# Kernel optimization log

Measured on AMD Instinct MI355X. Metric: run time of the kernel, lower is better.

Reference implementation:

```python
import jax, jax.numpy as jnp
import numpy as np
from jax import lax

B, N, D = 4, 2048, 1024
MAX_SEQ = 2048
GROUPS = 4  # math.gcd(1024, 4)
LN_EPS = 1e-5


def setup_inputs() -> dict:
    key = jax.random.key(0)
    ks = jax.random.split(key, 12)
    s = 0.02
    return {
        "x": jax.random.normal(ks[0], (B, N, D), jnp.float32),
        "Wq": jax.random.normal(ks[1], (D, D), jnp.float32) * s,
        "Wk": jax.random.normal(ks[2], (D, D), jnp.float32) * s,
        "Wv": jax.random.normal(ks[3], (D, D), jnp.float32) * s,
        "rel_bias": jax.random.normal(ks[4], (1, MAX_SEQ, MAX_SEQ), jnp.float32) * s,
        "conv_w": jax.random.normal(ks[5], (D, D // GROUPS, 3), jnp.float32) * s,
        "conv_b": jnp.zeros((D,), jnp.float32),
        "resg_w": jax.random.normal(ks[6], (D, D), jnp.float32) * s,
        "resg_b": jnp.zeros((D,), jnp.float32),
        "ln_g": jnp.ones((D,), jnp.float32),
        "ln_b": jnp.zeros((D,), jnp.float32),
        "fc1_w": jax.random.normal(ks[7], (D // 2, D), jnp.float32) * s,
        "fc1_b": jnp.zeros((D // 2,), jnp.float32),
        "fc2_w": jax.random.normal(ks[8], (1, D // 2), jnp.float32) * s,
        "fc2_b": jnp.zeros((1,), jnp.float32),
    }


def _forward(x, Wq, Wk, Wv, rel_bias, conv_w, conv_b, resg_w, resg_b,
             ln_g, ln_b, fc1_w, fc1_b, fc2_w, fc2_b):
    b, n, d = x.shape
    scale = 1.0 / jnp.sqrt(jnp.asarray(d, x.dtype))
    q = x @ Wq.T  # [b,n,dk]
    k = x @ Wk.T
    v = x @ Wv.T  # [b,n,dv]
    att = jnp.einsum("bqd,bkd->bqk", q, k) * scale + rel_bias[:, :n, :n]
    causal = jnp.tril(jnp.ones((n, n), bool))
    att = jnp.where(causal, att, jnp.asarray(-jnp.inf, att.dtype))
    att = jax.nn.softmax(att, axis=-1)  # dropout is identity at eval
    att_out = jnp.einsum("bqk,bkd->bqd", att, v)
    # grouped temporal conv over sequence dim: v [b,n,dv] -> NCH [b,dv,n]
    conv = lax.conv_general_dilated(
        v.transpose(0, 2, 1), conv_w, window_strides=(1,), padding=[(1, 1)],
        dimension_numbers=("NCH", "OIH", "NCH"), feature_group_count=GROUPS)
    conv = conv + conv_b[None, :, None]
    out = att_out + conv.transpose(0, 2, 1)
    res = jax.nn.sigmoid(out @ resg_w.T + resg_b)
    out = x + res * out
    mu = out.mean(-1, keepdims=True)
    var = out.var(-1, keepdims=True)
    out = (out - mu) * lax.rsqrt(var + LN_EPS) * ln_g + ln_b
    h = jax.nn.gelu(out @ fc1_w.T + fc1_b, approximate=False)
    return jax.nn.sigmoid(h @ fc2_w.T + fc2_b)


def reference(x, Wq, Wk, Wv, rel_bias, conv_w, conv_b, resg_w, resg_b,
              ln_g, ln_b, fc1_w, fc1_b, fc2_w, fc2_b):
    return _forward(x, Wq, Wk, Wv, rel_bias, conv_w, conv_b, resg_w, resg_b,
                    ln_g, ln_b, fc1_w, fc1_b, fc2_w, fc2_b)
```

## Files before the change

kernel.cpp:

```cpp
#include <hip/hip_runtime.h>
#include <math.h>

#define NSEQ 2048
#define DDIM 1024
#define BSZ  4
#define BM 128
#define BN 128
#define BK 32

typedef short bf16x8 __attribute__((ext_vector_type(8)));
typedef float f32x4 __attribute__((ext_vector_type(4)));
typedef unsigned int u32;
typedef unsigned short u16;

__device__ __forceinline__ u16 f2bf(float f) {
  union { float f; u32 u; } x; x.f = f;
  u32 r = x.u + 0x7FFFu + ((x.u >> 16) & 1u);
  return (u16)(r >> 16);
}
__device__ __forceinline__ float bf2f(u16 h) {
  union { u32 u; float f; } x; x.u = ((u32)h) << 16; return x.f;
}
__device__ __forceinline__ float sigmoidf_(float x) {
  return 1.0f / (1.0f + expf(-x));
}

__device__ __forceinline__ void async_copy16(const u16* g, u16* l) {
  __builtin_amdgcn_global_load_lds(
      (const __attribute__((address_space(1))) u32*)g,
      (__attribute__((address_space(3))) u32*)l, 16, 0, 0);
}

__device__ __forceinline__ void stage_tile(const u16* __restrict__ gsrc, size_t ld,
                                           int k0, u16* lds, int tid) {
  const int wave = tid >> 6, lane = tid & 63;
  const int rr = lane >> 2, cc = (lane & 3) << 3;
#pragma unroll
  for (int j = 0; j < 2; ++j) {
    const int c = j * 4 + wave;
    async_copy16(gsrc + (size_t)(c * 16 + rr) * ld + k0 + cc, lds + c * 512);
  }
}

__device__ __forceinline__ void mfma_step(const u16* Al, const u16* Bl,
                                          int wr, int wc, int l16, int quad,
                                          f32x4 acc[4][4]) {
  bf16x8 a[4], b[4];
#pragma unroll
  for (int i = 0; i < 4; ++i) {
    a[i] = *(const bf16x8*)(Al + (wr * 64 + i * 16 + l16) * BK + quad * 8);
    b[i] = *(const bf16x8*)(Bl + (wc * 64 + i * 16 + l16) * BK + quad * 8);
  }
#pragma unroll
  for (int i = 0; i < 4; ++i)
#pragma unroll
    for (int j = 0; j < 4; ++j)
      acc[i][j] = __builtin_amdgcn_mfma_f32_16x16x32_bf16(a[i], b[j], acc[i][j], 0, 0, 0);
}

__device__ __forceinline__ void zero_acc(f32x4 acc[4][4]) {
#pragma unroll
  for (int i = 0; i < 4; ++i)
#pragma unroll
    for (int j = 0; j < 4; ++j) {
      f32x4 z = {0.f, 0.f, 0.f, 0.f};
      acc[i][j] = z;
    }
}

__device__ __forceinline__ void gemm_loop(const u16* A, size_t lda,
                                          const u16* Bt, size_t ldb, int K,
                                          u16* Al, u16* Bl, int tid,
                                          int wr, int wc, int l16, int quad,
                                          f32x4 acc[4][4]) {
  for (int k0 = 0; k0 < K; k0 += BK) {
    __syncthreads();
    stage_tile(A, lda, k0, Al, tid);
    stage_tile(Bt, ldb, k0, Bl, tid);
    __syncthreads();
    mfma_step(Al, Bl, wr, wc, l16, quad, acc);
  }
}

__global__ __launch_bounds__(256) void k_cvt(const float* __restrict__ s,
                                             u16* __restrict__ d, int n4) {
  const int i = blockIdx.x * 256 + threadIdx.x;
  if (i < n4) {
    const float4 v = ((const float4*)s)[i];
    ushort4 o;
    o.x = f2bf(v.x); o.y = f2bf(v.y); o.z = f2bf(v.z); o.w = f2bf(v.w);
    ((ushort4*)d)[i] = o;
  }
}

__global__ __launch_bounds__(256) void k_cvtconv(const float* __restrict__ s,
                                                 u16* __restrict__ d) {
  const int o = blockIdx.x, i = threadIdx.x;
#pragma unroll
  for (int tap = 0; tap < 3; ++tap)
    d[(size_t)o * 768 + tap * 256 + i] = f2bf(s[(size_t)o * 768 + i * 3 + tap]);
}

__global__ __launch_bounds__(256) void k_zeropad(u16* __restrict__ vpad) {
  const int bb = blockIdx.x >> 1, which = blockIdx.x & 1;
  u16* row = vpad + (size_t)bb * 2050 * 1024 + (which ? (size_t)2049 * 1024 : 0);
  ushort4 z = {0, 0, 0, 0};
  ((ushort4*)row)[threadIdx.x] = z;
}

__global__ __launch_bounds__(256) void k_qkv(
    const u16* __restrict__ xb, const u16* __restrict__ Wqb,
    const u16* __restrict__ Wkb, const u16* __restrict__ Wvb,
    u16* __restrict__ qb, u16* __restrict__ kb, u16* __restrict__ vpad)
{
  __shared__ u16 Al[BM * BK], Bl[BN * BK];
  const int tid = threadIdx.x, z = blockIdx.z;
  const u16* W = (z == 0) ? Wqb : ((z == 1) ? Wkb : Wvb);
  const int row0 = blockIdx.x * BM, col0 = blockIdx.y * BN;
  const int lane = tid & 63, wave = tid >> 6;
  const int quad = lane >> 4, l16 = lane & 15, wr = wave >> 1, wc = wave & 1;
  f32x4 acc[4][4];
  zero_acc(acc);
  gemm_loop(xb + (size_t)row0 * DDIM, DDIM, W + (size_t)col0 * DDIM, DDIM, DDIM,
            Al, Bl, tid, wr, wc, l16, quad, acc);
#pragma unroll
  for (int mi = 0; mi < 4; ++mi)
#pragma unroll
    for (int r = 0; r < 4; ++r) {
      const int grow = row0 + wr * 64 + mi * 16 + quad * 4 + r;
#pragma unroll
      for (int ni = 0; ni < 4; ++ni) {
        const int gcol = col0 + wc * 64 + ni * 16 + l16;
        const u16 hv = f2bf(acc[mi][ni][r]);
        if (z == 2) {
          const int b = grow >> 11, t = grow & 2047;
          vpad[(size_t)b * 2050 * 1024 + 1024 + (size_t)t * 1024 + gcol] = hv;
        } else {
          (z == 0 ? qb : kb)[(size_t)grow * DDIM + gcol] = hv;
        }
      }
    }
}

__global__ __launch_bounds__(256) void k_vt(const u16* __restrict__ vpad,
                                            u16* __restrict__ vT)
{
  __shared__ u16 tile[64][72];
  const int t0 = blockIdx.x * 64, d0 = blockIdx.y * 64, b = blockIdx.z;
  const int tid = threadIdx.x;
  const u16* vb = vpad + (size_t)b * 2050 * 1024 + 1024;
#pragma unroll
  for (int p = 0; p < 4; ++p) {
    const int r = p * 16 + (tid >> 4), c = (tid & 15) << 2;
    const ushort4 v4 = *(const ushort4*)(vb + (size_t)(t0 + r) * 1024 + d0 + c);
    tile[r][c] = v4.x; tile[r][c + 1] = v4.y; tile[r][c + 2] = v4.z; tile[r][c + 3] = v4.w;
  }
  __syncthreads();
  u16* ob = vT + (size_t)b * DDIM * NSEQ;
#pragma unroll
  for (int p = 0; p < 4; ++p) {
    const int d = p * 16 + (tid >> 4), t = (tid & 15) << 2;
    ushort4 o;
    o.x = tile[t][d]; o.y = tile[t + 1][d]; o.z = tile[t + 2][d]; o.w = tile[t + 3][d];
    *(ushort4*)(ob + (size_t)(d0 + d) * NSEQ + t0 + t) = o;
  }
}

__global__ __launch_bounds__(256) void k_scores(
    const u16* __restrict__ qb, const u16* __restrict__ kb,
    const float* __restrict__ rb, u16* __restrict__ att)
{
  const int it = blockIdx.x, jt = blockIdx.y, b = blockIdx.z;
  if (jt > it) return;
  __shared__ u16 Al[BM * BK], Bl[BN * BK];
  const int tid = threadIdx.x;
  const int row0 = it * BM, col0 = jt * BN;
  const int lane = tid & 63, wave = tid >> 6;
  const int quad = lane >> 4, l16 = lane & 15, wr = wave >> 1, wc = wave & 1;
  f32x4 acc[4][4];
  zero_acc(acc);
  gemm_loop(qb + ((size_t)b * NSEQ + row0) * DDIM, DDIM,
            kb + ((size_t)b * NSEQ + col0) * DDIM, DDIM, DDIM,
            Al, Bl, tid, wr, wc, l16, quad, acc);
  u16* abase = att + (size_t)b * NSEQ * NSEQ;
#pragma unroll
  for (int mi = 0; mi < 4; ++mi)
#pragma unroll
    for (int r = 0; r < 4; ++r) {
      const int i = row0 + wr * 64 + mi * 16 + quad * 4 + r;
#pragma unroll
      for (int ni = 0; ni < 4; ++ni) {
        const int j = col0 + wc * 64 + ni * 16 + l16;
        abase[(size_t)i * NSEQ + j] =
            f2bf(acc[mi][ni][r] * 0.03125f + rb[(size_t)i * NSEQ + j]);
      }
    }
}

__global__ __launch_bounds__(256) void k_softmax(u16* __restrict__ att)
{
  const int i = blockIdx.x, b = blockIdx.y;
  u16* row = att + ((size_t)b * NSEQ + i) * NSEQ;
  const int valid = i + 1;
  const int wlen = ((i >> 7) + 1) << 7;
  const int tid = threadIdx.x;
  const int lane = tid & 63, wid = tid >> 6;

  float v[8];
  float m = -1e30f;
#pragma unroll
  for (int t = 0; t < 8; ++t) {
    const int idx = tid + (t << 8);
    v[t] = (idx < valid) ? bf2f(row[idx]) : -1e30f;
    m = fmaxf(m, v[t]);
  }
#pragma unroll
  for (int off = 32; off; off >>= 1) m = fmaxf(m, __shfl_xor(m, off));
  __shared__ float red[4];
  if (lane == 0) red[wid] = m;
  __syncthreads();
  m = fmaxf(fmaxf(red[0], red[1]), fmaxf(red[2], red[3]));
  __syncthreads();

  float s = 0.f;
#pragma unroll
  for (int t = 0; t < 8; ++t) {
    const int idx = tid + (t << 8);
    float e = (idx < valid) ? expf(v[t] - m) : 0.f;
    v[t] = e;
    s += e;
  }
#pragma unroll
  for (int off = 32; off; off >>= 1) s += __shfl_xor(s, off);
  if (lane == 0) red[wid] = s;
  __syncthreads();
  s = red[0] + red[1] + red[2] + red[3];
  const float inv = 1.0f / s;
#pragma unroll
  for (int t = 0; t < 8; ++t) {
    const int idx = tid + (t << 8);
    if (idx < wlen) row[idx] = f2bf(v[t] * inv);
  }
}

__global__ __launch_bounds__(256) void k_pv(
    const u16* __restrict__ att, const u16* __restrict__ vT,
    float* __restrict__ buf1)
{
  __shared__ u16 Al[BM * BK], Bl[BN * BK];
  const int it = blockIdx.x, nt = blockIdx.y, b = blockIdx.z;
  const int tid = threadIdx.x;
  const int row0 = it * BM, col0 = nt * BN;
  const int K = (it + 1) * BM;
  const int lane = tid & 63, wave = tid >> 6;
  const int quad = lane >> 4, l16 = lane & 15, wr = wave >> 1, wc = wave & 1;
  f32x4 acc[4][4];
  zero_acc(acc);
  gemm_loop(att + ((size_t)b * NSEQ + row0) * NSEQ, NSEQ,
            vT + ((size_t)b * DDIM + col0) * NSEQ, NSEQ, K,
            Al, Bl, tid, wr, wc, l16, quad, acc);
  float* obase = buf1 + (size_t)b * NSEQ * DDIM;
#pragma unroll
  for (int mi = 0; mi < 4; ++mi)
#pragma unroll
    for (int r = 0; r < 4; ++r) {
      const int grow = row0 + wr * 64 + mi * 16 + quad * 4 + r;
#pragma unroll
      for (int ni = 0; ni < 4; ++ni) {
        const int gcol = col0 + wc * 64 + ni * 16 + l16;
        obase[(size_t)grow * DDIM + gcol] = acc[mi][ni][r];
      }
    }
}

__global__ __launch_bounds__(256) void k_conv(
    const u16* __restrict__ vpad, const u16* __restrict__ cwp,
    const float* __restrict__ cb, float* __restrict__ buf1,
    u16* __restrict__ buf1b)
{
  __shared__ u16 Al[BM * BK], Bl[BN * BK];
  const int tid = threadIdx.x;
  const int row0 = blockIdx.x * BM;
  const int col0 = blockIdx.y * BN;
  const int g = col0 >> 8;
  const int b = row0 >> 11, t0 = row0 & 2047;
  const u16* vb = vpad + (size_t)b * 2050 * 1024 + 1024;
  const u16* Bbase = cwp + (size_t)col0 * 768;
  const int lane = tid & 63, wave = tid >> 6;
  const int quad = lane >> 4, l16 = lane & 15, wr = wave >> 1, wc = wave & 1;
  const int rr = lane >> 2, cc = (lane & 3) << 3;
  const int gch = g << 8;
  f32x4 acc[4][4];
  zero_acc(acc);
  for (int k0 = 0; k0 < 768; k0 += BK) {
    __syncthreads();
    const int tap = k0 >> 8;
    const int i0 = k0 & 255;
#pragma unroll
    for (int j = 0; j < 2; ++j) {
      const int c = j * 4 + wave;
      const int r = c * 16 + rr;
      async_copy16(vb + (size_t)(t0 + r - 1 + tap) * 1024 + gch + i0 + cc,
                   Al + c * 512);
    }
    stage_tile(Bbase, 768, k0, Bl, tid);
    __syncthreads();
    mfma_step(Al, Bl, wr, wc, l16, quad, acc);
  }
#pragma unroll
  for (int mi = 0; mi < 4; ++mi)
#pragma unroll
    for (int r = 0; r < 4; ++r) {
      const int grow = row0 + wr * 64 + mi * 16 + quad * 4 + r;
#pragma unroll
      for (int ni = 0; ni < 4; ++ni) {
        const int gcol = col0 + wc * 64 + ni * 16 + l16;
        const size_t idx = (size_t)grow * DDIM + gcol;
        const float val = buf1[idx] + cb[gcol] + acc[mi][ni][r];
        buf1[idx] = val;
        buf1b[idx] = f2bf(val);
      }
    }
}

__global__ __launch_bounds__(256) void k_resgate(
    const u16* __restrict__ buf1b, const u16* __restrict__ rwb,
    const float* __restrict__ rbias, const float* __restrict__ x,
    const float* __restrict__ buf1, float* __restrict__ buf2)
{
  __shared__ u16 Al[BM * BK], Bl[BN * BK];
  const int tid = threadIdx.x;
  const int row0 = blockIdx.x * BM, col0 = blockIdx.y * BN;
  const int lane = tid & 63, wave = tid >> 6;
  const int quad = lane >> 4, l16 = lane & 15, wr = wave >> 1, wc = wave & 1;
  f32x4 acc[4][4];
  zero_acc(acc);
  gemm_loop(buf1b + (size_t)row0 * DDIM, DDIM, rwb + (size_t)col0 * DDIM, DDIM,
            DDIM, Al, Bl, tid, wr, wc, l16, quad, acc);
#pragma unroll
  for (int mi = 0; mi < 4; ++mi)
#pragma unroll
    for (int r = 0; r < 4; ++r) {
      const int grow = row0 + wr * 64 + mi * 16 + quad * 4 + r;
#pragma unroll
      for (int ni = 0; ni < 4; ++ni) {
        const int gcol = col0 + wc * 64 + ni * 16 + l16;
        const size_t idx = (size_t)grow * DDIM + gcol;
        const float gate = sigmoidf_(acc[mi][ni][r] + rbias[gcol]);
        buf2[idx] = x[idx] + gate * buf1[idx];
      }
    }
}

__global__ __launch_bounds__(256) void k_ln(
    const float* __restrict__ buf, const float* __restrict__ gw,
    const float* __restrict__ gb, u16* __restrict__ outb)
{
  const int row = blockIdx.x;
  const float* p = buf + (size_t)row * DDIM;
  const int tid = threadIdx.x;
  const int lane = tid & 63, wid = tid >> 6;
  const int c = tid << 2;
  float4 val = *(const float4*)(p + c);
  float s = val.x + val.y + val.z + val.w;
  float s2 = val.x * val.x + val.y * val.y + val.z * val.z + val.w * val.w;
#pragma unroll
  for (int off = 32; off; off >>= 1) {
    s += __shfl_xor(s, off);
    s2 += __shfl_xor(s2, off);
  }
  __shared__ float r1[4], r2[4];
  if (lane == 0) { r1[wid] = s; r2[wid] = s2; }
  __syncthreads();
  s = r1[0] + r1[1] + r1[2] + r1[3];
  s2 = r2[0] + r2[1] + r2[2] + r2[3];
  const float mean = s * (1.0f / DDIM);
  const float var = s2 * (1.0f / DDIM) - mean * mean;
  const float rstd = rsqrtf(var + 1e-5f);
  const float4 g4 = *(const float4*)(gw + c);
  const float4 b4 = *(const float4*)(gb + c);
  ushort4 o;
  o.x = f2bf((val.x - mean) * rstd * g4.x + b4.x);
  o.y = f2bf((val.y - mean) * rstd * g4.y + b4.y);
  o.z = f2bf((val.z - mean) * rstd * g4.z + b4.z);
  o.w = f2bf((val.w - mean) * rstd * g4.w + b4.w);
  *(ushort4*)(outb + (size_t)row * DDIM + c) = o;
}

__global__ __launch_bounds__(256) void k_fc1(
    const u16* __restrict__ A, const u16* __restrict__ W,
    const float* __restrict__ bias, float* __restrict__ h)
{
  __shared__ u16 Al[BM * BK], Bl[BN * BK];
  const int tid = threadIdx.x;
  const int row0 = blockIdx.x * BM, col0 = blockIdx.y * BN;
  const int lane = tid & 63, wave = tid >> 6;
  const int quad = lane >> 4, l16 = lane & 15, wr = wave >> 1, wc = wave & 1;
  f32x4 acc[4][4];
  zero_acc(acc);
  gemm_loop(A + (size_t)row0 * DDIM, DDIM, W + (size_t)col0 * DDIM, DDIM, DDIM,
            Al, Bl, tid, wr, wc, l16, quad, acc);
#pragma unroll
  for (int mi = 0; mi < 4; ++mi)
#pragma unroll
    for (int r = 0; r < 4; ++r) {
      const int grow = row0 + wr * 64 + mi * 16 + quad * 4 + r;
#pragma unroll
      for (int ni = 0; ni < 4; ++ni) {
        const int gcol = col0 + wc * 64 + ni * 16 + l16;
        const float t = acc[mi][ni][r] + bias[gcol];
        h[(size_t)grow * 512 + gcol] = 0.5f * t * (1.0f + erff(t * 0.70710678118654752f));
      }
    }
}

__global__ __launch_bounds__(256) void k_fc2(
    const float* __restrict__ h, const float* __restrict__ w,
    const float* __restrict__ b2, float* __restrict__ out)
{
  const int r = blockIdx.x * 4 + (threadIdx.x >> 6);
  const int lane = threadIdx.x & 63;
  const float* hp = h + (size_t)r * 512;
  float s = 0.f;
#pragma unroll
  for (int t = 0; t < 8; ++t) {
    const int c = lane + t * 64;
    s = fmaf(hp[c], w[c], s);
  }
#pragma unroll
  for (int off = 32; off; off >>= 1) s += __shfl_xor(s, off);
  if (lane == 0) out[r] = sigmoidf_(s + b2[0]);
}

extern "C" void kernel_launch(void* const* d_in, const int* in_sizes, int n_in,
                              void* d_out, int out_size, void* d_ws, size_t ws_size,
                              hipStream_t stream) {
  const float* x    = (const float*)d_in[0];
  const float* Wq   = (const float*)d_in[1];
  const float* Wk   = (const float*)d_in[2];
  const float* Wv   = (const float*)d_in[3];
  const float* rb   = (const float*)d_in[4];
  const float* cw   = (const float*)d_in[5];
  const float* cb   = (const float*)d_in[6];
  const float* rw   = (const float*)d_in[7];
  const float* rbias= (const float*)d_in[8];
  const float* lng  = (const float*)d_in[9];
  const float* lnb  = (const float*)d_in[10];
  const float* f1w  = (const float*)d_in[11];
  const float* f1b  = (const float*)d_in[12];
  const float* f2w  = (const float*)d_in[13];
  const float* f2b  = (const float*)d_in[14];
  float* out = (float*)d_out;
  char* w8 = (char*)d_ws;

  u16* xb    = (u16*)(w8 + 0);
  u16* Wqb   = (u16*)(w8 + 16777216);
  u16* Wkb   = (u16*)(w8 + 18874368);
  u16* Wvb   = (u16*)(w8 + 20971520);
  u16* rwb   = (u16*)(w8 + 23068672);
  u16* f1wb  = (u16*)(w8 + 25165824);
  u16* cwp   = (u16*)(w8 + 26214400);
  u16* qb    = (u16*)(w8 + 27787264);
  u16* kb    = (u16*)(w8 + 44564480);
  u16* vpad  = (u16*)(w8 + 61341696);
  u16* vT    = (u16*)(w8 + 78131200);
  u16* att   = (u16*)(w8 + 94908416);
  float* buf1  = (float*)(w8 + 27787264);
  u16*   buf1b = (u16*)(w8 + 0);
  float* buf2  = (float*)(w8 + 94908416);
  u16*   ln16  = (u16*)(w8 + 78131200);
  float* h     = (float*)(w8 + 61341696);

  k_zeropad<<<dim3(8),    256, 0, stream>>>(vpad);
  k_cvt    <<<dim3(8192), 256, 0, stream>>>(x,   xb,   2097152);
  k_cvt    <<<dim3(1024), 256, 0, stream>>>(Wq,  Wqb,  262144);
  k_cvt    <<<dim3(1024), 256, 0, stream>>>(Wk,  Wkb,  262144);
  k_cvt    <<<dim3(1024), 256, 0, stream>>>(Wv,  Wvb,  262144);
  k_cvt    <<<dim3(1024), 256, 0, stream>>>(rw,  rwb,  262144);
  k_cvt    <<<dim3(512),  256, 0, stream>>>(f1w, f1wb, 131072);
  k_cvtconv<<<dim3(1024), 256, 0, stream>>>(cw, cwp);

  k_qkv    <<<dim3(64, 8, 3),  256, 0, stream>>>(xb, Wqb, Wkb, Wvb, qb, kb, vpad);
  k_vt     <<<dim3(32, 16, 4), 256, 0, stream>>>(vpad, vT);
  k_scores <<<dim3(16, 16, 4), 256, 0, stream>>>(qb, kb, rb, att);
  k_softmax<<<dim3(NSEQ, BSZ), 256, 0, stream>>>(att);
  k_pv     <<<dim3(16, 8, 4),  256, 0, stream>>>(att, vT, buf1);
  k_conv   <<<dim3(64, 8),     256, 0, stream>>>(vpad, cwp, cb, buf1, buf1b);
  k_resgate<<<dim3(64, 8),     256, 0, stream>>>(buf1b, rwb, rbias, x, buf1, buf2);
  k_ln     <<<dim3(BSZ * NSEQ),256, 0, stream>>>(buf2, lng, lnb, ln16);
  k_fc1    <<<dim3(64, 4),     256, 0, stream>>>(ln16, f1wb, f1b, h);
  k_fc2    <<<dim3(NSEQ),      256, 0, stream>>>(h, f2w, f2b, out);
}
```

Before: 444.8 us.

## Swizzle LDS tiles, merge prep kernels, keep attention scores in fp32

Applies an XOR swizzle to the k-group column used when staging tiles into LDS and when reading MFMA operands, so lanes spread across LDS banks instead of conflicting. Merges the seven conversion and zero-pad launches into one k_prep kernel to cut launch overhead. Stores the pre-softmax scores as fp32, presumably for accuracy, and writes bf16 probabilities to a separate buffer. That doubles the score write and read traffic and needs a reorganized workspace layout.

Measured after the change: 415.8 us. 1.07x faster.

```diff
diff --git a/kernel.cpp b/kernel.cpp
--- a/kernel.cpp
+++ b/kernel.cpp
@@ -34,7 +34,9 @@
 __device__ __forceinline__ void stage_tile(const u16* __restrict__ gsrc, size_t ld,
                                            int k0, u16* lds, int tid) {
   const int wave = tid >> 6, lane = tid & 63;
-  const int rr = lane >> 2, cc = (lane & 3) << 3;
+  const int rr = lane >> 2;
+  const int kg = (lane & 3) ^ ((lane >> 3) & 3);
+  const int cc = kg << 3;
 #pragma unroll
   for (int j = 0; j < 2; ++j) {
     const int c = j * 4 + wave;
@@ -45,11 +47,12 @@
 __device__ __forceinline__ void mfma_step(const u16* Al, const u16* Bl,
                                           int wr, int wc, int l16, int quad,
                                           f32x4 acc[4][4]) {
+  const int qs = (quad ^ ((l16 >> 1) & 3)) << 3;
   bf16x8 a[4], b[4];
 #pragma unroll
   for (int i = 0; i < 4; ++i) {
-    a[i] = *(const bf16x8*)(Al + (wr * 64 + i * 16 + l16) * BK + quad * 8);
-    b[i] = *(const bf16x8*)(Bl + (wc * 64 + i * 16 + l16) * BK + quad * 8);
+    a[i] = *(const bf16x8*)(Al + (wr * 64 + i * 16 + l16) * BK + qs);
+    b[i] = *(const bf16x8*)(Bl + (wc * 64 + i * 16 + l16) * BK + qs);
   }
 #pragma unroll
   for (int i = 0; i < 4; ++i)
@@ -82,30 +85,41 @@
   }
 }
 
-__global__ __launch_bounds__(256) void k_cvt(const float* __restrict__ s,
-                                             u16* __restrict__ d, int n4) {
-  const int i = blockIdx.x * 256 + threadIdx.x;
-  if (i < n4) {
-    const float4 v = ((const float4*)s)[i];
-    ushort4 o;
-    o.x = f2bf(v.x); o.y = f2bf(v.y); o.z = f2bf(v.z); o.w = f2bf(v.w);
-    ((ushort4*)d)[i] = o;
-  }
-}
-
-__global__ __launch_bounds__(256) void k_cvtconv(const float* __restrict__ s,
-                                                 u16* __restrict__ d) {
-  const int o = blockIdx.x, i = threadIdx.x;
-#pragma unroll
-  for (int tap = 0; tap < 3; ++tap)
-    d[(size_t)o * 768 + tap * 256 + i] = f2bf(s[(size_t)o * 768 + i * 3 + tap]);
-}
-
-__global__ __launch_bounds__(256) void k_zeropad(u16* __restrict__ vpad) {
-  const int bb = blockIdx.x >> 1, which = blockIdx.x & 1;
-  u16* row = vpad + (size_t)bb * 2050 * 1024 + (which ? (size_t)2049 * 1024 : 0);
-  ushort4 z = {0, 0, 0, 0};
-  ((ushort4*)row)[threadIdx.x] = z;
+__global__ __launch_bounds__(256) void k_prep(
+    const float* __restrict__ x,  const float* __restrict__ Wq,
+    const float* __restrict__ Wk, const float* __restrict__ Wv,
+    const float* __restrict__ rw, const float* __restrict__ f1w,
+    const float* __restrict__ cw,
+    u16* __restrict__ xb,  u16* __restrict__ Wqb, u16* __restrict__ Wkb,
+    u16* __restrict__ Wvb, u16* __restrict__ rwb, u16* __restrict__ f1wb,
+    u16* __restrict__ cwp, u16* __restrict__ vpad)
+{
+  const int blk = blockIdx.x, tid = threadIdx.x;
+  const float* s; u16* d; int base;
+  if (blk < 8192)       { s = x;   d = xb;   base = blk; }
+  else if (blk < 9216)  { s = Wq;  d = Wqb;  base = blk - 8192; }
+  else if (blk < 10240) { s = Wk;  d = Wkb;  base = blk - 9216; }
+  else if (blk < 11264) { s = Wv;  d = Wvb;  base = blk - 10240; }
+  else if (blk < 12288) { s = rw;  d = rwb;  base = blk - 11264; }
+  else if (blk < 12800) { s = f1w; d = f1wb; base = blk - 12288; }
+  else if (blk < 13824) {
+    const int o = blk - 12800, i = tid;
+#pragma unroll
+    for (int tap = 0; tap < 3; ++tap)
+      cwp[(size_t)o * 768 + tap * 256 + i] = f2bf(cw[(size_t)o * 768 + i * 3 + tap]);
+    return;
+  } else {
+    const int e = blk - 13824, bb = e >> 1, which = e & 1;
+    u16* row = vpad + (size_t)bb * 2050 * 1024 + (which ? (size_t)2049 * 1024 : 0);
+    ushort4 z = {0, 0, 0, 0};
+    ((ushort4*)row)[tid] = z;
+    return;
+  }
+  const int i = base * 256 + tid;
+  const float4 v = ((const float4*)s)[i];
+  ushort4 o;
+  o.x = f2bf(v.x); o.y = f2bf(v.y); o.z = f2bf(v.z); o.w = f2bf(v.w);
+  ((ushort4*)d)[i] = o;
 }
 
 __global__ __launch_bounds__(256) void k_qkv(
@@ -168,7 +182,7 @@
 
 __global__ __launch_bounds__(256) void k_scores(
     const u16* __restrict__ qb, const u16* __restrict__ kb,
-    const float* __restrict__ rb, u16* __restrict__ att)
+    const float* __restrict__ rb, float* __restrict__ att)
 {
   const int it = blockIdx.x, jt = blockIdx.y, b = blockIdx.z;
   if (jt > it) return;
@@ -182,7 +196,7 @@
   gemm_loop(qb + ((size_t)b * NSEQ + row0) * DDIM, DDIM,
             kb + ((size_t)b * NSEQ + col0) * DDIM, DDIM, DDIM,
             Al, Bl, tid, wr, wc, l16, quad, acc);
-  u16* abase = att + (size_t)b * NSEQ * NSEQ;
+  float* abase = att + (size_t)b * NSEQ * NSEQ;
 #pragma unroll
   for (int mi = 0; mi < 4; ++mi)
 #pragma unroll
@@ -192,15 +206,17 @@
       for (int ni = 0; ni < 4; ++ni) {
         const int j = col0 + wc * 64 + ni * 16 + l16;
         abase[(size_t)i * NSEQ + j] =
-            f2bf(acc[mi][ni][r] * 0.03125f + rb[(size_t)i * NSEQ + j]);
+            acc[mi][ni][r] * 0.03125f + rb[(size_t)i * NSEQ + j];
       }
     }
 }
 
-__global__ __launch_bounds__(256) void k_softmax(u16* __restrict__ att)
+__global__ __launch_bounds__(256) void k_softmax(const float* __restrict__ att,
+                                                 u16* __restrict__ attb)
 {
   const int i = blockIdx.x, b = blockIdx.y;
-  u16* row = att + ((size_t)b * NSEQ + i) * NSEQ;
+  const float* row = att + ((size_t)b * NSEQ + i) * NSEQ;
+  u16* orow = attb + ((size_t)b * NSEQ + i) * NSEQ;
   const int valid = i + 1;
   const int wlen = ((i >> 7) + 1) << 7;
   const int tid = threadIdx.x;
@@ -211,7 +227,7 @@
 #pragma unroll
   for (int t = 0; t < 8; ++t) {
     const int idx = tid + (t << 8);
-    v[t] = (idx < valid) ? bf2f(row[idx]) : -1e30f;
+    v[t] = (idx < valid) ? row[idx] : -1e30f;
     m = fmaxf(m, v[t]);
   }
 #pragma unroll
@@ -239,12 +255,12 @@
 #pragma unroll
   for (int t = 0; t < 8; ++t) {
     const int idx = tid + (t << 8);
-    if (idx < wlen) row[idx] = f2bf(v[t] * inv);
+    if (idx < wlen) orow[idx] = f2bf(v[t] * inv);
   }
 }
 
 __global__ __launch_bounds__(256) void k_pv(
-    const u16* __restrict__ att, const u16* __restrict__ vT,
+    const u16* __restrict__ attb, const u16* __restrict__ vT,
     float* __restrict__ buf1)
 {
   __shared__ u16 Al[BM * BK], Bl[BN * BK];
@@ -256,7 +272,7 @@
   const int quad = lane >> 4, l16 = lane & 15, wr = wave >> 1, wc = wave & 1;
   f32x4 acc[4][4];
   zero_acc(acc);
-  gemm_loop(att + ((size_t)b * NSEQ + row0) * NSEQ, NSEQ,
+  gemm_loop(attb + ((size_t)b * NSEQ + row0) * NSEQ, NSEQ,
             vT + ((size_t)b * DDIM + col0) * NSEQ, NSEQ, K,
             Al, Bl, tid, wr, wc, l16, quad, acc);
   float* obase = buf1 + (size_t)b * NSEQ * DDIM;
@@ -288,7 +304,9 @@
   const u16* Bbase = cwp + (size_t)col0 * 768;
   const int lane = tid & 63, wave = tid >> 6;
   const int quad = lane >> 4, l16 = lane & 15, wr = wave >> 1, wc = wave & 1;
-  const int rr = lane >> 2, cc = (lane & 3) << 3;
+  const int rr = lane >> 2;
+  const int kg = (lane & 3) ^ ((lane >> 3) & 3);
+  const int cc = kg << 3;
   const int gch = g << 8;
   f32x4 acc[4][4];
   zero_acc(acc);
@@ -463,28 +481,23 @@
   u16* qb    = (u16*)(w8 + 27787264);
   u16* kb    = (u16*)(w8 + 44564480);
   u16* vpad  = (u16*)(w8 + 61341696);
-  u16* vT    = (u16*)(w8 + 78131200);
-  u16* att   = (u16*)(w8 + 94908416);
-  float* buf1  = (float*)(w8 + 27787264);
+  u16* vT    = (u16*)(w8 + 78135296);
+  float* att = (float*)(w8 + 94912512);
+  u16*   attb  = (u16*)(w8 + 27787264);
+  float* buf1  = (float*)(w8 + 94912512);
   u16*   buf1b = (u16*)(w8 + 0);
-  float* buf2  = (float*)(w8 + 94908416);
-  u16*   ln16  = (u16*)(w8 + 78131200);
+  float* buf2  = (float*)(w8 + 128466944);
+  u16*   ln16  = (u16*)(w8 + 78135296);
   float* h     = (float*)(w8 + 61341696);
 
-  k_zeropad<<<dim3(8),    256, 0, stream>>>(vpad);
-  k_cvt    <<<dim3(8192), 256, 0, stream>>>(x,   xb,   2097152);
-  k_cvt    <<<dim3(1024), 256, 0, stream>>>(Wq,  Wqb,  262144);
-  k_cvt    <<<dim3(1024), 256, 0, stream>>>(Wk,  Wkb,  262144);
-  k_cvt    <<<dim3(1024), 256, 0, stream>>>(Wv,  Wvb,  262144);
-  k_cvt    <<<dim3(1024), 256, 0, stream>>>(rw,  rwb,  262144);
-  k_cvt    <<<dim3(512),  256, 0, stream>>>(f1w, f1wb, 131072);
-  k_cvtconv<<<dim3(1024), 256, 0, stream>>>(cw, cwp);
-
+  k_prep   <<<dim3(13832),     256, 0, stream>>>(x, Wq, Wk, Wv, rw, f1w, cw,
+                                                 xb, Wqb, Wkb, Wvb, rwb, f1wb,
+                                                 cwp, vpad);
   k_qkv    <<<dim3(64, 8, 3),  256, 0, stream>>>(xb, Wqb, Wkb, Wvb, qb, kb, vpad);
   k_vt     <<<dim3(32, 16, 4), 256, 0, stream>>>(vpad, vT);
   k_scores <<<dim3(16, 16, 4), 256, 0, stream>>>(qb, kb, rb, att);
-  k_softmax<<<dim3(NSEQ, BSZ), 256, 0, stream>>>(att);
-  k_pv     <<<dim3(16, 8, 4),  256, 0, stream>>>(att, vT, buf1);
+  k_softmax<<<dim3(NSEQ, BSZ), 256, 0, stream>>>(att, attb);
+  k_pv     <<<dim3(16, 8, 4),  256, 0, stream>>>(attb, vT, buf1);
   k_conv   <<<dim3(64, 8),     256, 0, stream>>>(vpad, cwp, cb, buf1, buf1b);
   k_resgate<<<dim3(64, 8),     256, 0, stream>>>(buf1b, rwb, rbias, x, buf1, buf2);
   k_ln     <<<dim3(BSZ * NSEQ),256, 0, stream>>>(buf2, lng, lnb, ln16);
```
